# Performance work log

Measured on AMD Instinct MI355X. Metric: run time of the kernel, lower is better.

The kernel has to match this reference:

```python
import jax, jax.numpy as jnp
import numpy as np

B = 1024
D = 768          # 2 * hidden_size
HID = 384        # hidden_size (split point for mu/sigma)
MLP_H = 300      # InfoNCE hidden size
LOG2PI = float(np.log(2.0 * np.pi))


def setup_inputs() -> dict:
    key = jax.random.key(0)
    ks = jax.random.split(key, 12)
    s = 0.02
    return {
        "zl": jax.random.normal(ks[0], (B, 20, D), jnp.float32),
        "zv": jax.random.normal(ks[1], (B, 36, D), jnp.float32),
        "fc_l_w": jax.random.normal(ks[2], (20,), jnp.float32) * s,
        "fc_l_b": jax.random.normal(ks[3], (), jnp.float32) * s,
        "fc_v_w": jax.random.normal(ks[4], (36,), jnp.float32) * s,
        "fc_v_b": jax.random.normal(ks[5], (), jnp.float32) * s,
        "W1": jax.random.normal(ks[6], (MLP_H, 2 * HID), jnp.float32) * s,
        "b1": jnp.zeros((MLP_H,), jnp.float32),
        "W2": jax.random.normal(ks[7], (1, MLP_H), jnp.float32) * s,
        "b2": jnp.zeros((1,), jnp.float32),
        "eps1": jax.random.normal(ks[8], (B, HID), jnp.float32),
        "eps2": jax.random.normal(ks[9], (B, HID), jnp.float32),
        "perm": jax.random.permutation(ks[10], B),
    }


def _log_prob(mu, sigma, x):
    # Independent(Normal(mu, sigma), 1).log_prob(x)
    z = (x - mu) / sigma
    return jnp.sum(-jnp.log(sigma) - 0.5 * LOG2PI - 0.5 * z * z, axis=-1)


def reference(zl, zv, fc_l_w, fc_l_b, fc_v_w, fc_v_b, W1, b1, W2, b2, eps1, eps2, perm):
    # fc over token dim: permute(0,2,1) @ Linear(20->1) -> [B, D]
    z1 = jnp.einsum('bsd,s->bd', zl, fc_l_w) + fc_l_b
    z2 = jnp.einsum('bsd,s->bd', zv, fc_v_w) + fc_v_b

    mu1, sig1 = z1[:, :HID], jax.nn.softplus(z1[:, HID:]) + 1e-7
    mu2, sig2 = z2[:, :HID], jax.nn.softplus(z2[:, HID:]) + 1e-7

    # rsample
    s1 = mu1 + sig1 * eps1  # [B, HID]
    s2 = mu2 + sig2 * eps2

    kl_1_2 = _log_prob(mu1, sig1, s1) - _log_prob(mu2, sig2, s1)
    kl_2_1 = _log_prob(mu2, sig2, s2) - _log_prob(mu1, sig1, s2)
    d_skl = jnp.mean(kl_1_2 + kl_2_1) / 2.0

    # InfoNCE(x=s1, y=s2): F(x,y) = softplus(relu([x,y]W1^T + b1) W2^T + b2)
    W1x, W1y = W1[:, :HID], W1[:, HID:]
    Ax = s1 @ W1x.T            # [B, MLP_H], x contribution
    By = s2 @ W1y.T            # [B, MLP_H], y contribution
    w2 = W2[0]                 # [MLP_H]

    # T0: matched pairs
    T0 = jax.nn.softplus(jax.nn.relu(Ax + By + b1) @ w2 + b2[0])  # [B]

    # T1[i, j] = F(x_j, y_perm[i]); tile via broadcasting instead of repeat+cat
    By_p = By[perm]                                             # [B, MLP_H]
    h = jax.nn.relu(Ax[None, :, :] + By_p[:, None, :] + b1)     # [B, B, MLP_H]
    T1 = jax.nn.softplus(h @ w2 + b2[0])                        # [B, B]

    lower_bound = T0.mean() - (jax.scipy.special.logsumexp(T1, axis=1).mean() - jnp.log(jnp.float32(B)))
    return d_skl - lower_bound
```

## Files before the change

kernel.cpp:

```cpp
#include <hip/hip_runtime.h>
#include <math.h>

#define BB   1024
#define DD   768
#define HIDV 384
#define MLPH 300
#define MLPP 320

typedef float v2f __attribute__((ext_vector_type(2)));

__device__ __forceinline__ float softplusf(float x) {
    return (x > 20.f) ? x : log1pf(expf(x));
}

__global__ void k_init(float* __restrict__ ws) {
    int i = blockIdx.x * 256 + threadIdx.x;
    if (i < 16 + BB) ws[i] = 0.f;
}

__global__ __launch_bounds__(384, 6) void k_rs(
    const float* __restrict__ zl, const float* __restrict__ zv,
    const float* __restrict__ wl, const float* __restrict__ blp,
    const float* __restrict__ wv, const float* __restrict__ bvp,
    const float* __restrict__ eps1, const float* __restrict__ eps2,
    float* __restrict__ s1, float* __restrict__ s2, float* __restrict__ accum)
{
    __shared__ float SG[768];
    __shared__ float MU2[384];
    __shared__ float pr[6];
    int tid = threadIdx.x;
    int b = blockIdx.x;
    int g = tid / 96;
    int c = tid - g * 96;

    const float4* p;
    if (g < 2) p = (const float4*)(zl + (size_t)b * 15360) + ((g & 1) * 96 + c);
    else       p = (const float4*)(zv + (size_t)b * 27648) + ((g & 1) * 96 + c);

    float acc[4] = {0.f, 0.f, 0.f, 0.f};
    if (g < 2) {
        #pragma unroll
        for (int t0 = 0; t0 < 20; t0 += 10) {
            float4 vb[10];
            #pragma unroll
            for (int u = 0; u < 10; ++u) vb[u] = p[(t0 + u) * 192];
            #pragma unroll
            for (int u = 0; u < 10; ++u) {
                float w = wl[t0 + u];
                acc[0] = fmaf(vb[u].x, w, acc[0]);
                acc[1] = fmaf(vb[u].y, w, acc[1]);
                acc[2] = fmaf(vb[u].z, w, acc[2]);
                acc[3] = fmaf(vb[u].w, w, acc[3]);
            }
        }
    } else {
        #pragma unroll
        for (int t0 = 0; t0 < 36; t0 += 9) {
            float4 vb[9];
            #pragma unroll
            for (int u = 0; u < 9; ++u) vb[u] = p[(t0 + u) * 192];
            #pragma unroll
            for (int u = 0; u < 9; ++u) {
                float w = wv[t0 + u];
                acc[0] = fmaf(vb[u].x, w, acc[0]);
                acc[1] = fmaf(vb[u].y, w, acc[1]);
                acc[2] = fmaf(vb[u].z, w, acc[2]);
                acc[3] = fmaf(vb[u].w, w, acc[3]);
            }
        }
    }

    float bl = blp[0], bv = bvp[0];

    if (g == 1) {
        float4 o;
        o.x = softplusf(acc[0] + bl) + 1e-7f;
        o.y = softplusf(acc[1] + bl) + 1e-7f;
        o.z = softplusf(acc[2] + bl) + 1e-7f;
        o.w = softplusf(acc[3] + bl) + 1e-7f;
        *(float4*)(SG + c * 4) = o;
    } else if (g == 2) {
        *(float4*)(MU2 + c * 4) =
            make_float4(acc[0] + bv, acc[1] + bv, acc[2] + bv, acc[3] + bv);
    } else if (g == 3) {
        float4 o;
        o.x = softplusf(acc[0] + bv) + 1e-7f;
        o.y = softplusf(acc[1] + bv) + 1e-7f;
        o.z = softplusf(acc[2] + bv) + 1e-7f;
        o.w = softplusf(acc[3] + bv) + 1e-7f;
        *(float4*)(SG + 384 + c * 4) = o;
    }
    __syncthreads();

    float con = 0.f;
    if (g == 0) {
        float4 e1v = ((const float4*)eps1)[b * 96 + c];
        float4 e2v = ((const float4*)eps2)[b * 96 + c];
        float4 g1 = *(const float4*)(SG + c * 4);
        float4 m2 = *(const float4*)(MU2 + c * 4);
        float4 g2 = *(const float4*)(SG + 384 + c * 4);
        float e1a[4] = {e1v.x, e1v.y, e1v.z, e1v.w};
        float e2a[4] = {e2v.x, e2v.y, e2v.z, e2v.w};
        float g1a[4] = {g1.x, g1.y, g1.z, g1.w};
        float g2a[4] = {g2.x, g2.y, g2.z, g2.w};
        float m2a[4] = {m2.x, m2.y, m2.z, m2.w};
        float s1o[4], s2o[4];
        #pragma unroll
        for (int j = 0; j < 4; ++j) {
            float mu1 = acc[j] + bl;
            float mu2 = m2a[j];
            float sg1 = g1a[j], sg2 = g2a[j];
            float e1 = e1a[j], e2 = e2a[j];
            float sv1 = fmaf(sg1, e1, mu1);
            float sv2 = fmaf(sg2, e2, mu2);
            s1o[j] = sv1; s2o[j] = sv2;
            float z12 = (sv1 - mu2) / sg2;
            float z21 = (sv2 - mu1) / sg1;
            con += -0.5f * (e1 * e1 + e2 * e2) + 0.5f * z12 * z12 + 0.5f * z21 * z21;
        }
        ((float4*)s1)[b * 96 + c] = make_float4(s1o[0], s1o[1], s1o[2], s1o[3]);
        ((float4*)s2)[b * 96 + c] = make_float4(s2o[0], s2o[1], s2o[2], s2o[3]);
    }

    #pragma unroll
    for (int m = 1; m < 64; m <<= 1) con += __shfl_xor(con, m);
    if ((tid & 63) == 0) pr[tid >> 6] = con;
    __syncthreads();
    if (tid == 0)
        atomicAdd(&accum[0], pr[0] + pr[1] + pr[2] + pr[3] + pr[4] + pr[5]);
}

__global__ __launch_bounds__(128) void k_gemm(
    const float* __restrict__ s1, const float* __restrict__ s2,
    const float* __restrict__ W1, const float* __restrict__ b1,
    float* __restrict__ Axb, float* __restrict__ By)
{
    __shared__ float Ss[64][34];
    __shared__ float Ws[64][18];
    int z = blockIdx.z;
    const float* S = z ? s2 : s1;
    float* Out = z ? By : Axb;
    int wofs = z ? HIDV : 0;
    int b0 = blockIdx.x * 32;
    int n0 = blockIdx.y * 16;
    int tid = threadIdx.x;
    int srow = tid & 31, sq = tid >> 5;
    int wrow = tid >> 3, wq = tid & 7;
    int nrow = n0 + wrow;
    int bp = tid & 15, np = tid >> 4;

    float4 ps[4], pw[2];
    auto ld = [&](int hc) {
        #pragma unroll
        for (int u = 0; u < 4; ++u)
            ps[u] = *(const float4*)&S[(b0 + srow) * HIDV + hc + (sq + 4 * u) * 4];
        #pragma unroll
        for (int u = 0; u < 2; ++u)
            pw[u] = (nrow < MLPH)
                ? *(const float4*)&W1[nrow * DD + wofs + hc + (wq + 8 * u) * 4]
                : make_float4(0.f, 0.f, 0.f, 0.f);
    };
    ld(0);
    v2f acc[2];
    acc[0] = (v2f){0.f, 0.f}; acc[1] = (v2f){0.f, 0.f};

    for (int ch = 0; ch < 6; ++ch) {
        __syncthreads();
        #pragma unroll
        for (int u = 0; u < 4; ++u) {
            int hq = (sq + 4 * u) * 4;
            Ss[hq + 0][srow] = ps[u].x; Ss[hq + 1][srow] = ps[u].y;
            Ss[hq + 2][srow] = ps[u].z; Ss[hq + 3][srow] = ps[u].w;
        }
        #pragma unroll
        for (int u = 0; u < 2; ++u) {
            int hq = (wq + 8 * u) * 4;
            Ws[hq + 0][wrow] = pw[u].x; Ws[hq + 1][wrow] = pw[u].y;
            Ws[hq + 2][wrow] = pw[u].z; Ws[hq + 3][wrow] = pw[u].w;
        }
        __syncthreads();
        if (ch < 5) ld((ch + 1) * 64);
        #pragma unroll
        for (int h = 0; h < 64; ++h) {
            v2f sv = *(const v2f*)&Ss[h][bp * 2];
            v2f wv = *(const v2f*)&Ws[h][np * 2];
            acc[0] = __builtin_elementwise_fma((v2f){sv.x, sv.x}, wv, acc[0]);
            acc[1] = __builtin_elementwise_fma((v2f){sv.y, sv.y}, wv, acc[1]);
        }
    }
    #pragma unroll
    for (int i = 0; i < 2; ++i) {
        int bb = b0 + bp * 2 + i;
        int n = n0 + np * 2;
        float r0 = 0.f, r1 = 0.f;
        if (n < MLPH)     r0 = acc[i].x + (z ? 0.f : b1[n]);
        if (n + 1 < MLPH) r1 = acc[i].y + (z ? 0.f : b1[n + 1]);
        *(v2f*)&Out[bb * MLPP + n] = (v2f){r0, r1};
    }
}

__global__ __launch_bounds__(256) void k_t0(
    const float* __restrict__ Axb, const float* __restrict__ By,
    const float* __restrict__ W2, const float* __restrict__ b2,
    float* __restrict__ accum)
{
    int tid = threadIdx.x;
    int w = tid >> 6, l = tid & 63;
    int b = blockIdx.x * 4 + w;
    const float4* A4 = (const float4*)(Axb + b * MLPP);
    const float4* B4 = (const float4*)(By + b * MLPP);
    const float4* W4 = (const float4*)W2;
    float t = 0.f;
    {
        float4 a = A4[l], bb = B4[l], ww = W4[l];
        t = fmaf(fmaxf(a.x + bb.x, 0.f), ww.x, t);
        t = fmaf(fmaxf(a.y + bb.y, 0.f), ww.y, t);
        t = fmaf(fmaxf(a.z + bb.z, 0.f), ww.z, t);
        t = fmaf(fmaxf(a.w + bb.w, 0.f), ww.w, t);
    }
    if (l < 11) {
        float4 a = A4[64 + l], bb = B4[64 + l], ww = W4[64 + l];
        t = fmaf(fmaxf(a.x + bb.x, 0.f), ww.x, t);
        t = fmaf(fmaxf(a.y + bb.y, 0.f), ww.y, t);
        t = fmaf(fmaxf(a.z + bb.z, 0.f), ww.z, t);
        t = fmaf(fmaxf(a.w + bb.w, 0.f), ww.w, t);
    }
    #pragma unroll
    for (int m = 1; m < 64; m <<= 1) t += __shfl_xor(t, m);
    if (l == 0) atomicAdd(&accum[1], softplusf(t + b2[0]));
}

__global__ __launch_bounds__(256) void k_pairs(
    const float* __restrict__ Axb, const float* __restrict__ By,
    const int* __restrict__ perm, const float* __restrict__ W2,
    const float* __restrict__ b2, float* __restrict__ sumexp)
{
    __shared__ float As[64][34];
    __shared__ float Bs[64][34];
    __shared__ float w2s[MLPP];
    int tid = threadIdx.x;
    int j0 = blockIdx.x * 32;
    int i0 = blockIdx.y * 32;
    for (int t = tid; t < MLPP; t += 256) w2s[t] = (t < MLPH) ? W2[t] : 0.f;
    int row = tid & 31;
    int q   = tid >> 5;
    int jp = tid & 15;
    int ip = tid >> 4;
    int prow = perm[i0 + row];

    float4 pa[2], pb[2];
    auto ld = [&](int kc) {
        #pragma unroll
        for (int u = 0; u < 2; ++u) {
            int kq = (q + 8 * u) * 4;
            pa[u] = *(const float4*)&Axb[(j0 + row) * MLPP + kc + kq];
            pb[u] = *(const float4*)&By[prow * MLPP + kc + kq];
        }
    };
    ld(0);
    v2f acc2[2];
    acc2[0] = (v2f){0.f, 0.f};
    acc2[1] = (v2f){0.f, 0.f};

    for (int ch = 0; ch < 5; ++ch) {
        __syncthreads();
        #pragma unroll
        for (int u = 0; u < 2; ++u) {
            int kq = (q + 8 * u) * 4;
            As[kq + 0][row] = pa[u].x; As[kq + 1][row] = pa[u].y;
            As[kq + 2][row] = pa[u].z; As[kq + 3][row] = pa[u].w;
            Bs[kq + 0][row] = pb[u].x; Bs[kq + 1][row] = pb[u].y;
            Bs[kq + 2][row] = pb[u].z; Bs[kq + 3][row] = pb[u].w;
        }
        __syncthreads();
        if (ch < 4) ld((ch + 1) * 64);
        int kc = ch * 64;
        #pragma unroll
        for (int k = 0; k < 64; ++k) {
            float w = w2s[kc + k];
            v2f wv2 = (v2f){w, w};
            v2f av = *(const v2f*)&As[k][jp * 2];
            v2f bv = *(const v2f*)&Bs[k][ip * 2];
            v2f t0v = av + (v2f){bv.x, bv.x};
            t0v = __builtin_elementwise_max(t0v, (v2f){0.f, 0.f});
            acc2[0] = __builtin_elementwise_fma(t0v, wv2, acc2[0]);
            v2f t1v = av + (v2f){bv.y, bv.y};
            t1v = __builtin_elementwise_max(t1v, (v2f){0.f, 0.f});
            acc2[1] = __builtin_elementwise_fma(t1v, wv2, acc2[1]);
        }
    }
    float b2v = b2[0];
    #pragma unroll
    for (int i2 = 0; i2 < 2; ++i2) {
        float ssum = (1.f + expf(acc2[i2].x + b2v)) + (1.f + expf(acc2[i2].y + b2v));
        ssum += __shfl_xor(ssum, 1);
        ssum += __shfl_xor(ssum, 2);
        ssum += __shfl_xor(ssum, 4);
        ssum += __shfl_xor(ssum, 8);
        if (jp == 0) atomicAdd(&sumexp[i0 + ip * 2 + i2], ssum);
    }
}

__global__ __launch_bounds__(256) void k_final(
    const float* __restrict__ accum, const float* __restrict__ sumexp,
    float* __restrict__ out)
{
    int tid = threadIdx.x;
    float s = 0.f;
    for (int i = tid; i < BB; i += 256) s += logf(sumexp[i]);
    #pragma unroll
    for (int m = 1; m < 64; m <<= 1) s += __shfl_xor(s, m);
    __shared__ float red[4];
    if ((tid & 63) == 0) red[tid >> 6] = s;
    __syncthreads();
    if (tid == 0) {
        float lse_mean = (red[0] + red[1] + red[2] + red[3]) / (float)BB;
        float d_skl = accum[0] / (2.f * (float)BB);
        float t0_mean = accum[1] / (float)BB;
        float lower = t0_mean - (lse_mean - logf((float)BB));
        out[0] = d_skl - lower;
    }
}

extern "C" void kernel_launch(void* const* d_in, const int* in_sizes, int n_in,
                              void* d_out, int out_size, void* d_ws, size_t ws_size,
                              hipStream_t stream)
{
    const float* zl     = (const float*)d_in[0];
    const float* zv     = (const float*)d_in[1];
    const float* fc_l_w = (const float*)d_in[2];
    const float* fc_l_b = (const float*)d_in[3];
    const float* fc_v_w = (const float*)d_in[4];
    const float* fc_v_b = (const float*)d_in[5];
    const float* W1     = (const float*)d_in[6];
    const float* b1     = (const float*)d_in[7];
    const float* W2     = (const float*)d_in[8];
    const float* b2     = (const float*)d_in[9];
    const float* eps1   = (const float*)d_in[10];
    const float* eps2   = (const float*)d_in[11];
    const int*   perm   = (const int*)d_in[12];
    float* out = (float*)d_out;

    float* ws     = (float*)d_ws;
    float* accum  = ws;
    float* sumexp = ws + 16;
    float* s1     = ws + 16 + BB;
    float* s2     = s1 + BB * HIDV;
    float* Axb    = s2 + BB * HIDV;
    float* By     = Axb + BB * MLPP;

    k_init<<<5, 256, 0, stream>>>(ws);
    k_rs<<<BB, 384, 0, stream>>>(zl, zv, fc_l_w, fc_l_b, fc_v_w, fc_v_b,
                                 eps1, eps2, s1, s2, accum);
    k_gemm<<<dim3(32, 20, 2), 128, 0, stream>>>(s1, s2, W1, b1, Axb, By);
    k_t0<<<256, 256, 0, stream>>>(Axb, By, W2, b2, accum);
    k_pairs<<<dim3(32, 32), 256, 0, stream>>>(Axb, By, perm, W2, b2, sumexp);
    k_final<<<1, 256, 0, stream>>>(accum, sumexp, out);
}
```

Measured before the change: 354.9 us.

## Enlarge register tiles in gemm and pairwise kernels to 4x4 per thread

Doubles the block tiles of the projection GEMM (32x16 to 64x32) and the pairwise kernel (32x32 to 64x64), so each thread now computes a 4x4 output micro-tile from float4 LDS reads instead of 2x2. The goal is more FMAs per shared-memory load and less staging traffic per output. It also moves the padded W2 vector into workspace, written by the init kernel, and k_pairs reads it from global memory instead of filling shared memory. The cost is more registers and fewer blocks: k_pairs drops from 1024 to 256 blocks, which may underfill the 256 CUs on MI355X.

```diff
diff --git a/kernel.cpp b/kernel.cpp
--- a/kernel.cpp
+++ b/kernel.cpp
@@ -13,9 +13,13 @@
     return (x > 20.f) ? x : log1pf(expf(x));
 }
 
-__global__ void k_init(float* __restrict__ ws) {
+__global__ void k_init(float* __restrict__ ws, const float* __restrict__ W2) {
     int i = blockIdx.x * 256 + threadIdx.x;
     if (i < 16 + BB) ws[i] = 0.f;
+    else if (i < 16 + BB + MLPP) {
+        int k = i - 16 - BB;
+        ws[i] = (k < MLPH) ? W2[k] : 0.f;
+    }
 }
 
 __global__ __launch_bounds__(384, 6) void k_rs(
@@ -135,67 +139,80 @@
     const float* __restrict__ W1, const float* __restrict__ b1,
     float* __restrict__ Axb, float* __restrict__ By)
 {
-    __shared__ float Ss[64][34];
-    __shared__ float Ws[64][18];
+    __shared__ float Ss[64][68];
+    __shared__ float Ws[64][36];
     int z = blockIdx.z;
     const float* S = z ? s2 : s1;
     float* Out = z ? By : Axb;
     int wofs = z ? HIDV : 0;
-    int b0 = blockIdx.x * 32;
-    int n0 = blockIdx.y * 16;
-    int tid = threadIdx.x;
-    int srow = tid & 31, sq = tid >> 5;
-    int wrow = tid >> 3, wq = tid & 7;
+    int b0 = blockIdx.x * 64;
+    int n0 = blockIdx.y * 32;
+    int tid = threadIdx.x;
+    int srow = tid >> 1, sq8 = (tid & 1) * 8;
+    int wrow = tid >> 2, wq4 = (tid & 3) * 4;
     int nrow = n0 + wrow;
     int bp = tid & 15, np = tid >> 4;
 
-    float4 ps[4], pw[2];
+    float4 ps[8], pw[4];
     auto ld = [&](int hc) {
         #pragma unroll
+        for (int u = 0; u < 8; ++u)
+            ps[u] = *(const float4*)&S[(b0 + srow) * HIDV + hc + (sq8 + u) * 4];
+        #pragma unroll
         for (int u = 0; u < 4; ++u)
-            ps[u] = *(const float4*)&S[(b0 + srow) * HIDV + hc + (sq + 4 * u) * 4];
-        #pragma unroll
-        for (int u = 0; u < 2; ++u)
             pw[u] = (nrow < MLPH)
-                ? *(const float4*)&W1[nrow * DD + wofs + hc + (wq + 8 * u) * 4]
+                ? *(const float4*)&W1[nrow * DD + wofs + hc + (wq4 + u) * 4]
                 : make_float4(0.f, 0.f, 0.f, 0.f);
     };
     ld(0);
-    v2f acc[2];
-    acc[0] = (v2f){0.f, 0.f}; acc[1] = (v2f){0.f, 0.f};
+    v2f acc[4][2];
+    #pragma unroll
+    for (int i = 0; i < 4; ++i) { acc[i][0] = (v2f){0.f,0.f}; acc[i][1] = (v2f){0.f,0.f}; }
 
     for (int ch = 0; ch < 6; ++ch) {
         __syncthreads();
         #pragma unroll
+        for (int u = 0; u < 8; ++u) {
+            int h4 = (sq8 + u) * 4;
+            Ss[h4 + 0][srow] = ps[u].x; Ss[h4 + 1][srow] = ps[u].y;
+            Ss[h4 + 2][srow] = ps[u].z; Ss[h4 + 3][srow] = ps[u].w;
+        }
+        #pragma unroll
         for (int u = 0; u < 4; ++u) {
-            int hq = (sq + 4 * u) * 4;
-            Ss[hq + 0][srow] = ps[u].x; Ss[hq + 1][srow] = ps[u].y;
-            Ss[hq + 2][srow] = ps[u].z; Ss[hq + 3][srow] = ps[u].w;
-        }
-        #pragma unroll
-        for (int u = 0; u < 2; ++u) {
-            int hq = (wq + 8 * u) * 4;
-            Ws[hq + 0][wrow] = pw[u].x; Ws[hq + 1][wrow] = pw[u].y;
-            Ws[hq + 2][wrow] = pw[u].z; Ws[hq + 3][wrow] = pw[u].w;
+            int h4 = (wq4 + u) * 4;
+            Ws[h4 + 0][wrow] = pw[u].x; Ws[h4 + 1][wrow] = pw[u].y;
+            Ws[h4 + 2][wrow] = pw[u].z; Ws[h4 + 3][wrow] = pw[u].w;
         }
         __syncthreads();
         if (ch < 5) ld((ch + 1) * 64);
         #pragma unroll
         for (int h = 0; h < 64; ++h) {
-            v2f sv = *(const v2f*)&Ss[h][bp * 2];
-            v2f wv = *(const v2f*)&Ws[h][np * 2];
-            acc[0] = __builtin_elementwise_fma((v2f){sv.x, sv.x}, wv, acc[0]);
-            acc[1] = __builtin_elementwise_fma((v2f){sv.y, sv.y}, wv, acc[1]);
-        }
-    }
-    #pragma unroll
-    for (int i = 0; i < 2; ++i) {
-        int bb = b0 + bp * 2 + i;
-        int n = n0 + np * 2;
-        float r0 = 0.f, r1 = 0.f;
-        if (n < MLPH)     r0 = acc[i].x + (z ? 0.f : b1[n]);
-        if (n + 1 < MLPH) r1 = acc[i].y + (z ? 0.f : b1[n + 1]);
-        *(v2f*)&Out[bb * MLPP + n] = (v2f){r0, r1};
+            float4 sv = *(const float4*)&Ss[h][bp * 4];
+            float4 wv = *(const float4*)&Ws[h][np * 4];
+            v2f w01 = (v2f){wv.x, wv.y}, w23 = (v2f){wv.z, wv.w};
+            float sa[4] = {sv.x, sv.y, sv.z, sv.w};
+            #pragma unroll
+            for (int i = 0; i < 4; ++i) {
+                v2f sb = (v2f){sa[i], sa[i]};
+                acc[i][0] = __builtin_elementwise_fma(sb, w01, acc[i][0]);
+                acc[i][1] = __builtin_elementwise_fma(sb, w23, acc[i][1]);
+            }
+        }
+    }
+    int nbase = n0 + np * 4;
+    #pragma unroll
+    for (int i = 0; i < 4; ++i) {
+        int bb = b0 + bp * 4 + i;
+        float va[4] = {acc[i][0].x, acc[i][0].y, acc[i][1].x, acc[i][1].y};
+        float o[4];
+        #pragma unroll
+        for (int c = 0; c < 4; ++c) {
+            int n = nbase + c;
+            float v = va[c];
+            if (!z && n < MLPH) v += b1[n];
+            o[c] = (n < MLPH) ? v : 0.f;
+        }
+        *(float4*)&Out[bb * MLPP + nbase] = make_float4(o[0], o[1], o[2], o[3]);
     }
 }
 
@@ -232,41 +249,39 @@
 
 __global__ __launch_bounds__(256) void k_pairs(
     const float* __restrict__ Axb, const float* __restrict__ By,
-    const int* __restrict__ perm, const float* __restrict__ W2,
+    const int* __restrict__ perm, const float* __restrict__ w2p,
     const float* __restrict__ b2, float* __restrict__ sumexp)
 {
-    __shared__ float As[64][34];
-    __shared__ float Bs[64][34];
-    __shared__ float w2s[MLPP];
-    int tid = threadIdx.x;
-    int j0 = blockIdx.x * 32;
-    int i0 = blockIdx.y * 32;
-    for (int t = tid; t < MLPP; t += 256) w2s[t] = (t < MLPH) ? W2[t] : 0.f;
-    int row = tid & 31;
-    int q   = tid >> 5;
+    __shared__ float As[64][68];
+    __shared__ float Bs[64][68];
+    int tid = threadIdx.x;
+    int j0 = blockIdx.x * 64;
+    int i0 = blockIdx.y * 64;
+    int row = tid & 63;
+    int q   = tid >> 6;
     int jp = tid & 15;
     int ip = tid >> 4;
     int prow = perm[i0 + row];
 
-    float4 pa[2], pb[2];
+    float4 pa[4], pb[4];
     auto ld = [&](int kc) {
         #pragma unroll
-        for (int u = 0; u < 2; ++u) {
-            int kq = (q + 8 * u) * 4;
+        for (int u = 0; u < 4; ++u) {
+            int kq = (q + 4 * u) * 4;
             pa[u] = *(const float4*)&Axb[(j0 + row) * MLPP + kc + kq];
             pb[u] = *(const float4*)&By[prow * MLPP + kc + kq];
         }
     };
     ld(0);
-    v2f acc2[2];
-    acc2[0] = (v2f){0.f, 0.f};
-    acc2[1] = (v2f){0.f, 0.f};
+    v2f acc2[4][2];
+    #pragma unroll
+    for (int i = 0; i < 4; ++i) { acc2[i][0] = (v2f){0.f,0.f}; acc2[i][1] = (v2f){0.f,0.f}; }
 
     for (int ch = 0; ch < 5; ++ch) {
         __syncthreads();
         #pragma unroll
-        for (int u = 0; u < 2; ++u) {
-            int kq = (q + 8 * u) * 4;
+        for (int u = 0; u < 4; ++u) {
+            int kq = (q + 4 * u) * 4;
             As[kq + 0][row] = pa[u].x; As[kq + 1][row] = pa[u].y;
             As[kq + 2][row] = pa[u].z; As[kq + 3][row] = pa[u].w;
             Bs[kq + 0][row] = pb[u].x; Bs[kq + 1][row] = pb[u].y;
@@ -277,27 +292,34 @@
         int kc = ch * 64;
         #pragma unroll
         for (int k = 0; k < 64; ++k) {
-            float w = w2s[kc + k];
+            float w = w2p[kc + k];
             v2f wv2 = (v2f){w, w};
-            v2f av = *(const v2f*)&As[k][jp * 2];
-            v2f bv = *(const v2f*)&Bs[k][ip * 2];
-            v2f t0v = av + (v2f){bv.x, bv.x};
-            t0v = __builtin_elementwise_max(t0v, (v2f){0.f, 0.f});
-            acc2[0] = __builtin_elementwise_fma(t0v, wv2, acc2[0]);
-            v2f t1v = av + (v2f){bv.y, bv.y};
-            t1v = __builtin_elementwise_max(t1v, (v2f){0.f, 0.f});
-            acc2[1] = __builtin_elementwise_fma(t1v, wv2, acc2[1]);
+            float4 af = *(const float4*)&As[k][jp * 4];
+            float4 bf = *(const float4*)&Bs[k][ip * 4];
+            v2f alo = (v2f){af.x, af.y}, ahi = (v2f){af.z, af.w};
+            float ba[4] = {bf.x, bf.y, bf.z, bf.w};
+            #pragma unroll
+            for (int i = 0; i < 4; ++i) {
+                v2f bc = (v2f){ba[i], ba[i]};
+                v2f t0v = alo + bc;
+                t0v = __builtin_elementwise_max(t0v, (v2f){0.f, 0.f});
+                acc2[i][0] = __builtin_elementwise_fma(t0v, wv2, acc2[i][0]);
+                v2f t1v = ahi + bc;
+                t1v = __builtin_elementwise_max(t1v, (v2f){0.f, 0.f});
+                acc2[i][1] = __builtin_elementwise_fma(t1v, wv2, acc2[i][1]);
+            }
         }
     }
     float b2v = b2[0];
     #pragma unroll
-    for (int i2 = 0; i2 < 2; ++i2) {
-        float ssum = (1.f + expf(acc2[i2].x + b2v)) + (1.f + expf(acc2[i2].y + b2v));
+    for (int i = 0; i < 4; ++i) {
+        float ssum = (1.f + expf(acc2[i][0].x + b2v)) + (1.f + expf(acc2[i][0].y + b2v))
+                   + (1.f + expf(acc2[i][1].x + b2v)) + (1.f + expf(acc2[i][1].y + b2v));
         ssum += __shfl_xor(ssum, 1);
         ssum += __shfl_xor(ssum, 2);
         ssum += __shfl_xor(ssum, 4);
         ssum += __shfl_xor(ssum, 8);
-        if (jp == 0) atomicAdd(&sumexp[i0 + ip * 2 + i2], ssum);
+        if (jp == 0) atomicAdd(&sumexp[i0 + ip * 4 + i], ssum);
     }
 }
 
@@ -344,16 +366,17 @@
     float* ws     = (float*)d_ws;
     float* accum  = ws;
     float* sumexp = ws + 16;
-    float* s1     = ws + 16 + BB;
+    float* w2p    = ws + 16 + BB;
+    float* s1     = w2p + MLPP;
     float* s2     = s1 + BB * HIDV;
     float* Axb    = s2 + BB * HIDV;
     float* By     = Axb + BB * MLPP;
 
-    k_init<<<5, 256, 0, stream>>>(ws);
+    k_init<<<6, 256, 0, stream>>>(ws, W2);
     k_rs<<<BB, 384, 0, stream>>>(zl, zv, fc_l_w, fc_l_b, fc_v_w, fc_v_b,
                                  eps1, eps2, s1, s2, accum);
-    k_gemm<<<dim3(32, 20, 2), 128, 0, stream>>>(s1, s2, W1, b1, Axb, By);
+    k_gemm<<<dim3(16, 10, 2), 128, 0, stream>>>(s1, s2, W1, b1, Axb, By);
     k_t0<<<256, 256, 0, stream>>>(Axb, By, W2, b2, accum);
-    k_pairs<<<dim3(32, 32), 256, 0, stream>>>(Axb, By, perm, W2, b2, sumexp);
+    k_pairs<<<dim3(16, 16), 256, 0, stream>>>(Axb, By, perm, w2p, b2, sumexp);
     k_final<<<1, 256, 0, stream>>>(accum, sumexp, out);
 }
```

Result: faster. 309.1 us (-12.9%).
